# Optimization experiments

Hardware: AMD Instinct MI355X
Metric: run time of the kernel (lower is better)

The kernel has to match this reference:

```python
import jax, jax.numpy as jnp
import numpy as np

STRIDE = 16
HF = WF = 160
IM_H = IM_W = STRIDE * HF  # 2560
A = 15
PRE_NMS = 3000
RPN_KEEP = 300
RPN_NMS_TH = 0.7
OBJ_TH = 0.2
MIN_SIZE = 8.0
G = 7
OUT_DIM = 10
S = 2  # bilinear samples per bin per axis
NUM_FG = 3
SCORE_TH = 0.3
RCNN_NMS_TH = 0.5
FINAL_KEEP = 100
BBOX_STD = jnp.array([0.1, 0.1, 0.2, 0.2], jnp.float32)


def gen_anchors():
    base = 16.0
    anchors = []
    for r in [0.5, 1.0, 2.0]:
        for s in [2.0, 4.0, 8.0, 16.0, 32.0]:
            size = base * s
            w = size * np.sqrt(1.0 / r)
            h = size * np.sqrt(r)
            anchors.append([-w / 2, -h / 2, w / 2, h / 2])
    return jnp.asarray(np.array(anchors, np.float32))  # [A,4]


def decode_boxes(anchors, deltas):
    d = deltas * BBOX_STD
    wa = anchors[..., 2] - anchors[..., 0] + 1.0
    ha = anchors[..., 3] - anchors[..., 1] + 1.0
    cxa = anchors[..., 0] + 0.5 * wa
    cya = anchors[..., 1] + 0.5 * ha
    cx = d[..., 0] * wa + cxa
    cy = d[..., 1] * ha + cya
    w = wa * jnp.exp(jnp.minimum(d[..., 2], 4.0))
    h = ha * jnp.exp(jnp.minimum(d[..., 3], 4.0))
    boxes = jnp.stack([cx - 0.5 * w, cy - 0.5 * h, cx + 0.5 * w, cy + 0.5 * h], -1)
    hi = jnp.array([IM_W - 1.0, IM_H - 1.0, IM_W - 1.0, IM_H - 1.0], jnp.float32)
    return jnp.clip(boxes, 0.0, hi)


def greedy_nms(boxes, scores, iou_th, keep_n):
    # scores <= 0 means pre-suppressed/invalid
    N = boxes.shape[0]
    areas = jnp.maximum(boxes[:, 2] - boxes[:, 0] + 1.0, 0.0) * jnp.maximum(boxes[:, 3] - boxes[:, 1] + 1.0, 0.0)

    def body(k, st):
        sup, keep = st
        s = jnp.where(sup, -1e30, scores)
        i = jnp.argmax(s)
        valid = s[i] > -1e29
        keep = keep.at[k].set(jnp.where(valid, i.astype(jnp.int32), N))
        bi = boxes[i]
        ix1 = jnp.maximum(bi[0], boxes[:, 0]); iy1 = jnp.maximum(bi[1], boxes[:, 1])
        ix2 = jnp.minimum(bi[2], boxes[:, 2]); iy2 = jnp.minimum(bi[3], boxes[:, 3])
        inter = jnp.maximum(ix2 - ix1 + 1.0, 0.0) * jnp.maximum(iy2 - iy1 + 1.0, 0.0)
        iou = inter / jnp.maximum(areas[i] + areas - inter, 1e-6)
        sup2 = (sup | (iou > iou_th)).at[i].set(True)
        sup = jnp.where(valid, sup2, sup)
        return sup, keep

    sup0 = scores <= 0.0
    keep0 = jnp.full((keep_n,), N, jnp.int32)
    _, keep = jax.lax.fori_loop(0, keep_n, body, (sup0, keep0))
    return keep, keep < N


def rpn_proposal(rpn_cls, rpn_bbox):
    fg = rpn_cls[0, A:]                                           # [A,HF,WF] objectness
    deltas = rpn_bbox[0].reshape(A, 4, HF, WF).transpose(0, 2, 3, 1)  # [A,HF,WF,4]
    anchors = gen_anchors()
    sx = jnp.arange(WF, dtype=jnp.float32) * STRIDE
    sy = jnp.arange(HF, dtype=jnp.float32) * STRIDE
    gx, gy = jnp.meshgrid(sx, sy)                                 # [HF,WF]
    shift = jnp.stack([gx, gy, gx, gy], -1)                       # [HF,WF,4]
    all_anchors = anchors[:, None, None, :] + shift[None]         # [A,HF,WF,4]
    boxes = decode_boxes(all_anchors, deltas).reshape(-1, 4)      # [A*HF*WF,4]
    scores = fg.reshape(-1)
    w = boxes[:, 2] - boxes[:, 0] + 1.0
    h = boxes[:, 3] - boxes[:, 1] + 1.0
    ok = (w >= MIN_SIZE) & (h >= MIN_SIZE) & (scores > OBJ_TH)
    scores = jnp.where(ok, scores, 0.0)
    sc, idx = jax.lax.top_k(scores, PRE_NMS)
    bx = boxes[idx]
    keep, valid = greedy_nms(bx, sc, RPN_NMS_TH, RPN_KEEP)
    bxp = jnp.concatenate([bx, jnp.zeros((1, 4), bx.dtype)], 0)
    rois = bxp[keep] * valid[:, None].astype(bx.dtype)            # [RPN_KEEP,4]
    return rois, valid


def psroi_align(ft, rois, valid):
    # ft [490,HF,WF]; position-sensitive channel = (c*G+ph)*G+pw
    x1 = rois[:, 0] / STRIDE; y1 = rois[:, 1] / STRIDE
    x2 = rois[:, 2] / STRIDE; y2 = rois[:, 3] / STRIDE
    bw = jnp.maximum(x2 - x1, 0.1) / G
    bh = jnp.maximum(y2 - y1, 0.1) / G
    frac = (jnp.arange(S, dtype=jnp.float32) + 0.5) / S           # [S]
    grid = jnp.arange(G, dtype=jnp.float32)[None, :, None] + frac[None, None, :]  # [1,G,S]
    ys = jnp.clip(y1[:, None, None] + grid * bh[:, None, None], 0.0, HF - 1.0)    # [R,G,S]
    xs = jnp.clip(x1[:, None, None] + grid * bw[:, None, None], 0.0, WF - 1.0)
    y0 = jnp.floor(ys); x0 = jnp.floor(xs)
    wy = ys - y0; wx = xs - x0
    y0i = y0.astype(jnp.int32); x0i = x0.astype(jnp.int32)
    y1i = jnp.minimum(y0i + 1, HF - 1); x1i = jnp.minimum(x0i + 1, WF - 1)
    chan = (jnp.arange(OUT_DIM)[:, None, None] * G + jnp.arange(G)[None, :, None]) * G + jnp.arange(G)[None, None, :]
    ch = chan[None, :, :, :, None, None]                          # [1,C,G,G,1,1]
    Y0 = y0i[:, None, :, None, :, None]; Y1 = y1i[:, None, :, None, :, None]
    X0 = x0i[:, None, None, :, None, :]; X1 = x1i[:, None, None, :, None, :]
    WY = wy[:, None, :, None, :, None]; WX = wx[:, None, None, :, None, :]
    v00 = ft[ch, Y0, X0]; v01 = ft[ch, Y0, X1]
    v10 = ft[ch, Y1, X0]; v11 = ft[ch, Y1, X1]                    # [R,C,G,G,S,S]
    val = v00 * (1 - WY) * (1 - WX) + v01 * (1 - WY) * WX + v10 * WY * (1 - WX) + v11 * WY * WX
    pooled = val.mean(axis=(4, 5))                                # [R,C,G,G]
    return pooled * valid[:, None, None, None].astype(pooled.dtype)


def rcnn_proposal(cls_sm, bbox_pred, rois, valid):
    R = rois.shape[0]
    deltas = bbox_pred.reshape(R, 4, 4)[:, 1:, :]                 # [R,3,4] fg classes
    boxes = decode_boxes(rois[:, None, :], deltas)                # [R,3,4]
    scores = cls_sm[:, 1:] * valid[:, None].astype(cls_sm.dtype)  # [R,3]
    scores = jnp.where(scores > SCORE_TH, scores, 0.0)
    fb = boxes.reshape(-1, 4)
    fs = scores.reshape(-1)
    labels = jnp.tile(jnp.arange(1, NUM_FG + 1, dtype=jnp.float32), (R,))
    keep, kv = greedy_nms(fb, fs, RCNN_NMS_TH, FINAL_KEEP)
    fbp = jnp.concatenate([fb, jnp.zeros((1, 4), fb.dtype)], 0)
    fsp = jnp.concatenate([fs, jnp.zeros((1,), fs.dtype)], 0)
    flp = jnp.concatenate([labels, jnp.zeros((1,), labels.dtype)], 0)
    out = jnp.concatenate([fbp[keep], fsp[keep][:, None], flp[keep][:, None]], -1)  # [FINAL_KEEP,6]
    return out * kv[:, None].astype(out.dtype)


def setup_inputs() -> dict:
    key = jax.random.key(0)
    ks = jax.random.split(key, 9)
    return {
        'rpn_cls_prob_reshape': jax.random.uniform(ks[0], (1, 2 * A, HF, WF), jnp.float32),
        'rpn_bbox_pred': jax.random.normal(ks[1], (1, 4 * A, HF, WF), jnp.float32),
        'ft_add_left_right': jax.random.normal(ks[2], (1, OUT_DIM * G * G, HF, WF), jnp.float32),
        'w1': jax.random.normal(ks[3], (490, 2048), jnp.float32) * 0.02,
        'b1': jnp.zeros((2048,), jnp.float32),
        'w_cls': jax.random.normal(ks[4], (2048, 4), jnp.float32) * 0.02,
        'b_cls': jnp.zeros((4,), jnp.float32),
        'w_bbox': jax.random.normal(ks[5], (2048, 16), jnp.float32) * 0.02,
        'b_bbox': jnp.zeros((16,), jnp.float32),
    }


def reference(rpn_cls_prob_reshape, rpn_bbox_pred, ft_add_left_right, w1, b1, w_cls, b_cls, w_bbox, b_bbox):
    rois, valid = rpn_proposal(rpn_cls_prob_reshape, rpn_bbox_pred)
    pooled = psroi_align(ft_add_left_right[0], rois, valid)       # [R,10,7,7]
    feats = pooled.reshape(-1, OUT_DIM * G * G)                   # [R,490]
    h = jax.nn.relu(feats @ w1 + b1)
    cls_sm = jax.nn.softmax(h @ w_cls + b_cls, axis=-1)
    bbox = h @ w_bbox + b_bbox
    return rcnn_proposal(cls_sm, bbox, rois, valid)
```

## Files before the change

### kernel.cpp

```cpp
#include <hip/hip_runtime.h>
#include <stdint.h>

#define HF_ 160
#define WF_ 160
#define HFW 25600
#define A_N 15
#define NTOT 384000
#define PRE_N 3000
#define KEEP_N 300
#define FEAT_N 490
#define HID_N 2048
#define RC_N 900
#define FIN_N 100
#define TIE_CAP 1024
#define NW 47
#define NSTAGE 320
#define RNW 15
#define FC1_MT 10
#define FC1_KP 496
#define ZN (65536 * 2 + 32)

__constant__ float c_hw[15] = {
  22.627416997969522f, 45.254833995939045f, 90.509667991878090f, 181.01933598375618f, 362.03867196751236f,
  16.0f, 32.0f, 64.0f, 128.0f, 256.0f,
  11.313708498984761f, 22.627416997969522f, 45.254833995939045f, 90.509667991878090f, 181.01933598375618f
};
__constant__ float c_hh[15] = {
  11.313708498984761f, 22.627416997969522f, 45.254833995939045f, 90.509667991878090f, 181.01933598375618f,
  16.0f, 32.0f, 64.0f, 128.0f, 256.0f,
  22.627416997969522f, 45.254833995939045f, 90.509667991878090f, 181.01933598375618f, 362.03867196751236f
};

__device__ __forceinline__ void decode_one(
    float ax1, float ay1, float ax2, float ay2,
    float dx, float dy, float dw, float dh,
    float& ox1, float& oy1, float& ox2, float& oy2)
{
#pragma clang fp contract(off)
  float wa = (ax2 - ax1) + 1.0f;
  float ha = (ay2 - ay1) + 1.0f;
  float cxa = ax1 + 0.5f * wa;
  float cya = ay1 + 0.5f * ha;
  float d0 = dx * 0.1f;
  float d1 = dy * 0.1f;
  float d2 = dw * 0.2f;
  float d3 = dh * 0.2f;
  float cx = d0 * wa + cxa;
  float cy = d1 * ha + cya;
  float w  = wa * expf(fminf(d2, 4.0f));
  float h  = ha * expf(fminf(d3, 4.0f));
  float x1 = cx - 0.5f * w;
  float y1 = cy - 0.5f * h;
  float x2 = cx + 0.5f * w;
  float y2 = cy + 0.5f * h;
  ox1 = fminf(fmaxf(x1, 0.0f), 2559.0f);
  oy1 = fminf(fmaxf(y1, 0.0f), 2559.0f);
  ox2 = fminf(fmaxf(x2, 0.0f), 2559.0f);
  oy2 = fminf(fmaxf(y2, 0.0f), 2559.0f);
}

__device__ __forceinline__ float iou_ref(
    float ax1, float ay1, float ax2, float ay2, float areaA,
    float bx1, float by1, float bx2, float by2)
{
#pragma clang fp contract(off)
  float ix1 = fmaxf(ax1, bx1);
  float iy1 = fmaxf(ay1, by1);
  float ix2 = fminf(ax2, bx2);
  float iy2 = fminf(ay2, by2);
  float iw = fmaxf((ix2 - ix1) + 1.0f, 0.0f);
  float ih = fmaxf((iy2 - iy1) + 1.0f, 0.0f);
  float inter = iw * ih;
  float areaB = fmaxf((bx2 - bx1) + 1.0f, 0.0f) * fmaxf((by2 - by1) + 1.0f, 0.0f);
  float den = fmaxf(areaA + areaB - inter, 1e-6f);
  return inter / den;
}

__global__ void k_decode_score(const float* __restrict__ cls,
                               const float* __restrict__ bbox,
                               float* __restrict__ scores,
                               uint32_t* __restrict__ histzero)
{
  int e = blockIdx.x * 256 + threadIdx.x;
  if (e < ZN) histzero[e] = 0u;
  if (e >= NTOT) return;
  int a   = e / HFW;
  int rem = e - a * HFW;
  int i   = rem / WF_;
  int j   = rem - i * WF_;
  float score = cls[(A_N + a) * HFW + rem];
  float gx = (float)(j * 16);
  float gy = (float)(i * 16);
  float hw = c_hw[a], hh = c_hh[a];
  float dx = bbox[(a * 4 + 0) * HFW + rem];
  float dy = bbox[(a * 4 + 1) * HFW + rem];
  float dw = bbox[(a * 4 + 2) * HFW + rem];
  float dh = bbox[(a * 4 + 3) * HFW + rem];
  float x1, y1, x2, y2;
  decode_one(gx - hw, gy - hh, gx + hw, gy + hh, dx, dy, dw, dh, x1, y1, x2, y2);
  float bw, bh;
  {
#pragma clang fp contract(off)
    bw = (x2 - x1) + 1.0f;
    bh = (y2 - y1) + 1.0f;
  }
  bool ok = (bw >= 8.0f) && (bh >= 8.0f) && (score > 0.2f);
  scores[e] = ok ? score : 0.0f;
}

__global__ void k_hist_hi(const float* __restrict__ scores, uint32_t* __restrict__ hist)
{
  __shared__ uint32_t lh[512];
  int t = threadIdx.x;
  for (int i = t; i < 512; i += 256) lh[i] = 0u;
  __syncthreads();
  int e = blockIdx.x * 256 + t;
  if (e < NTOT) {
    float s = scores[e];
    if (s > 0.0f) {
      uint32_t b = __float_as_uint(s) >> 16;
      if (b >= 0x3E00u && b < 0x4000u) atomicAdd(&lh[b - 0x3E00u], 1u);
      else atomicAdd(&hist[b], 1u);
    }
  }
  __syncthreads();
  for (int i = t; i < 512; i += 256) {
    uint32_t v = lh[i];
    if (v) atomicAdd(&hist[0x3E00u + i], v);
  }
}

__global__ void __launch_bounds__(1024) k_findbin1(const uint32_t* __restrict__ hist,
                                                   uint32_t* __restrict__ meta)
{
  __shared__ uint32_t sfx[1024];
  __shared__ int s_chunk;
  __shared__ uint32_t s_exc;
  int t = threadIdx.x;
  if (t == 0) s_chunk = -1;
  const uint32_t* hp = hist + t * 64;
  uint32_t s = 0;
#pragma unroll
  for (int b = 0; b < 64; b++) s += hp[b];
  sfx[t] = s;
  __syncthreads();
  for (int d = 1; d < 1024; d <<= 1) {
    uint32_t v = (t + d < 1024) ? sfx[t + d] : 0u;
    __syncthreads();
    sfx[t] += v;
    __syncthreads();
  }
  uint32_t inc = sfx[t];
  uint32_t exc = (t < 1023) ? sfx[t + 1] : 0u;
  if (exc < (uint32_t)PRE_N && inc >= (uint32_t)PRE_N) { s_chunk = t; s_exc = exc; }
  __syncthreads();
  int c = s_chunk;
  if (c < 0) {
    if (t == 0) { meta[0] = 0u; meta[1] = 0u; meta[2] = 1u; }
    return;
  }
  if (t < 64) {
    uint32_t h = hist[c * 64 + t];
    uint32_t v = h;
#pragma unroll
    for (int d = 1; d < 64; d <<= 1) {
      uint32_t o = (uint32_t)__shfl_down((int)v, d);
      v += (t + d < 64) ? o : 0u;
    }
    uint32_t before = s_exc + (v - h);
    if (before < (uint32_t)PRE_N && before + h >= (uint32_t)PRE_N) {
      meta[0] = (uint32_t)(c * 64 + t);
      meta[1] = (uint32_t)PRE_N - before;
      meta[2] = 0u;
    }
  }
}

__global__ void k_hist_lo(const float* __restrict__ scores,
                          const uint32_t* __restrict__ meta,
                          uint32_t* __restrict__ hist2)
{
  if (meta[2]) return;
  uint32_t B1 = meta[0];
  int e = blockIdx.x * 256 + threadIdx.x;
  if (e >= NTOT) return;
  float s = scores[e];
  if (s <= 0.0f) return;
  uint32_t bits = __float_as_uint(s);
  if ((bits >> 16) == B1) atomicAdd(&hist2[bits & 0xFFFFu], 1u);
}

__global__ void __launch_bounds__(1024) k_findT(const uint32_t* __restrict__ hist2,
                                                uint32_t* __restrict__ meta)
{
  if (meta[2]) { if (threadIdx.x == 0) meta[3] = 0u; return; }
  __shared__ uint32_t sfx[1024];
  __shared__ int s_chunk;
  __shared__ uint32_t s_exc;
  int t = threadIdx.x;
  if (t == 0) s_chunk = -1;
  uint32_t K = meta[1];
  const uint32_t* hp = hist2 + t * 64;
  uint32_t s = 0;
#pragma unroll
  for (int b = 0; b < 64; b++) s += hp[b];
  sfx[t] = s;
  __syncthreads();
  for (int d = 1; d < 1024; d <<= 1) {
    uint32_t v = (t + d < 1024) ? sfx[t + d] : 0u;
    __syncthreads();
    sfx[t] += v;
    __syncthreads();
  }
  uint32_t inc = sfx[t];
  uint32_t exc = (t < 1023) ? sfx[t + 1] : 0u;
  if (exc < K && inc >= K) { s_chunk = t; s_exc = exc; }
  __syncthreads();
  int c = s_chunk;
  if (c < 0) { if (t == 0) meta[3] = 0u; return; }
  if (t < 64) {
    uint32_t h = hist2[c * 64 + t];
    uint32_t v = h;
#pragma unroll
    for (int d = 1; d < 64; d <<= 1) {
      uint32_t o = (uint32_t)__shfl_down((int)v, d);
      v += (t + d < 64) ? o : 0u;
    }
    uint32_t before = s_exc + (v - h);
    if (before < K && before + h >= K)
      meta[3] = (meta[0] << 16) | (uint32_t)(c * 64 + t);
  }
}

__global__ void k_compact(const float* __restrict__ scores,
                          const uint32_t* __restrict__ meta,
                          uint64_t* __restrict__ gt,
                          uint64_t* __restrict__ tie,
                          uint32_t* __restrict__ cnts)
{
  int e = blockIdx.x * 256 + threadIdx.x;
  if (e >= NTOT) return;
  float s = scores[e];
  if (s <= 0.0f) return;
  uint32_t bits = __float_as_uint(s);
  uint32_t T = meta[3];
  uint64_t key = ((uint64_t)bits << 32) | (uint32_t)(~(uint32_t)e);
  if (bits > T) {
    uint32_t p = atomicAdd(&cnts[0], 1u);
    if (p < (uint32_t)PRE_N) gt[p] = key;
  } else if (bits == T) {
    uint32_t p = atomicAdd(&cnts[1], 1u);
    if (p < (uint32_t)TIE_CAP) tie[p] = key;
  }
}

__global__ void __launch_bounds__(256) k_rank_gather(
    const uint64_t* __restrict__ gt,
    const uint64_t* __restrict__ tie,
    const uint32_t* __restrict__ cnts,
    const float* __restrict__ bbox,
    float* __restrict__ bxx1, float* __restrict__ bxy1,
    float* __restrict__ bxx2, float* __restrict__ bxy2)
{
  __shared__ uint64_t keys[4096];
  int t = threadIdx.x;
  uint32_t ngt = min(cnts[0], (uint32_t)PRE_N);
  uint32_t nte = min(cnts[1], (uint32_t)TIE_CAP);
  uint32_t M = ngt + nte;
  for (int s = t; s < 4096; s += 256) {
    uint64_t k = 0;
    if ((uint32_t)s < ngt) k = gt[s];
    else if ((uint32_t)s < M) k = tie[s - ngt];
    keys[s] = k;
  }
  __syncthreads();
  int e = blockIdx.x * 256 + t;
  uint64_t my = keys[e];
  if (my == 0) return;
  int r = 0;
#pragma unroll 4
  for (int j = 0; j < 4096; j += 4) {
    uint64_t k0 = keys[j + 0];
    uint64_t k1 = keys[j + 1];
    uint64_t k2 = keys[j + 2];
    uint64_t k3 = keys[j + 3];
    r += (k0 > my) ? 1 : 0;
    r += (k1 > my) ? 1 : 0;
    r += (k2 > my) ? 1 : 0;
    r += (k3 > my) ? 1 : 0;
  }
  if (r >= PRE_N) return;
  int idx = (int)(~(uint32_t)(my & 0xFFFFFFFFull));
  int a   = idx / HFW;
  int rem = idx - a * HFW;
  int i   = rem / WF_;
  int j   = rem - i * WF_;
  float gx = (float)(j * 16);
  float gy = (float)(i * 16);
  float hw = c_hw[a], hh = c_hh[a];
  float dx = bbox[(a * 4 + 0) * HFW + rem];
  float dy = bbox[(a * 4 + 1) * HFW + rem];
  float dw = bbox[(a * 4 + 2) * HFW + rem];
  float dh = bbox[(a * 4 + 3) * HFW + rem];
  float x1, y1, x2, y2;
  decode_one(gx - hw, gy - hh, gx + hw, gy + hh, dx, dy, dw, dh, x1, y1, x2, y2);
  bxx1[r] = x1; bxy1[r] = y1; bxx2[r] = x2; bxy2[r] = y2;
}

__global__ void __launch_bounds__(256) k_iou_mask(
    const float* __restrict__ bxx1, const float* __restrict__ bxy1,
    const float* __restrict__ bxx2, const float* __restrict__ bxy2,
    uint64_t* __restrict__ rowmask, uint64_t* __restrict__ diag)
{
  __shared__ float s1[PRE_N], s2[PRE_N], s3[PRE_N], s4[PRE_N];
  int t = threadIdx.x;
  for (int e = t; e < PRE_N; e += 256) {
    s1[e] = bxx1[e]; s2[e] = bxy1[e]; s3[e] = bxx2[e]; s4[e] = bxy2[e];
  }
  __syncthreads();
  int task = blockIdx.x * 256 + t;
  if (task >= PRE_N * NW) return;
  int row = task / NW;
  int w   = task - row * NW;
  if ((w + 1) * 64 <= row) {
    rowmask[(size_t)row * NW + w] = 0;
    return;
  }
  float ax1 = s1[row], ay1 = s2[row], ax2 = s3[row], ay2 = s4[row];
  float areaA;
  {
#pragma clang fp contract(off)
    areaA = fmaxf((ax2 - ax1) + 1.0f, 0.0f) * fmaxf((ay2 - ay1) + 1.0f, 0.0f);
  }
  int j0 = w << 6;
  uint64_t bits = 0;
  for (int off = 0; off < 64; off++) {
    int jj = (off + t) & 63;
    int j = j0 + jj;
    if (j < PRE_N) {
      float iou = iou_ref(ax1, ay1, ax2, ay2, areaA, s1[j], s2[j], s3[j], s4[j]);
      if (iou > 0.7f) bits |= 1ull << jj;
    }
  }
  rowmask[(size_t)row * NW + w] = bits;
  if (w == (row >> 6)) diag[row] = bits;
}

__global__ void __launch_bounds__(256) k_rpn_scan(
    const float* __restrict__ bxx1, const float* __restrict__ bxy1,
    const float* __restrict__ bxx2, const float* __restrict__ bxy2,
    const uint32_t* __restrict__ cnts,
    const uint64_t* __restrict__ rowmask,
    const uint64_t* __restrict__ diag,
    float* __restrict__ rois, uint32_t* __restrict__ valid)
{
  __shared__ uint64_t rowstage[NSTAGE * NW];
  __shared__ uint64_t sdiag[PRE_N];
  __shared__ int keepIdx[KEEP_N];
  __shared__ int s_nkeep;
  int t = threadIdx.x;
  for (int e = t; e < NSTAGE * NW; e += 256) rowstage[e] = rowmask[e];
  for (int e = t; e < PRE_N; e += 256) sdiag[e] = diag[e];
  __syncthreads();
  if (t < 64) {
    int lane = t;
    uint32_t Mp = min(cnts[0] + min(cnts[1], (uint32_t)TIE_CAP), (uint32_t)PRE_N);
    uint64_t sup = 0, pend = 0;
    int nk = 0;
    int nwords = (int)((Mp + 63u) >> 6);
    for (int w = 0; w < nwords && nk < KEEP_N; w++) {
      sup |= pend; pend = 0;
      uint64_t cw = (uint64_t)__shfl((unsigned long long)sup, w);
      int lim = (int)Mp - (w << 6);
      uint64_t range = (lim >= 64) ? ~0ull : ((1ull << lim) - 1ull);
      uint64_t rem = (~cw) & range;
      while (rem && nk < KEEP_N) {
        int b = __builtin_ctzll(rem);
        int i = (w << 6) + b;
        if (lane == 0) keepIdx[nk] = i;
        nk++;
        uint64_t roww = sdiag[i];
        uint64_t rowl = 0;
        if (lane < NW)
          rowl = (i < NSTAGE) ? rowstage[i * NW + lane]
                              : rowmask[(size_t)i * NW + lane];
        sup |= pend;
        pend = rowl;
        rem &= ~(roww | (1ull << b));
      }
    }
    sup |= pend;
    if (lane == 0) s_nkeep = nk;
  }
  __syncthreads();
  int nk2 = s_nkeep;
  for (int k = t; k < nk2; k += 256) {
    int i = keepIdx[k];
    rois[k * 4 + 0] = bxx1[i];
    rois[k * 4 + 1] = bxy1[i];
    rois[k * 4 + 2] = bxx2[i];
    rois[k * 4 + 3] = bxy2[i];
    valid[k] = 1u;
  }
  for (int e = nk2 * 4 + t; e < KEEP_N * 4; e += 256) rois[e] = 0.0f;
  for (int e = nk2 + t; e < KEEP_N; e += 256) valid[e] = 0u;
}

__global__ void __launch_bounds__(512) k_psroi(const float* __restrict__ ft,
                                               const float* __restrict__ rois,
                                               const uint32_t* __restrict__ valid,
                                               float* __restrict__ feats)
{
#pragma clang fp contract(off)
  int r = blockIdx.x;
  int t = threadIdx.x;
  if (t >= FEAT_N) return;
  float x1 = rois[r * 4 + 0] * 0.0625f;
  float y1 = rois[r * 4 + 1] * 0.0625f;
  float x2 = rois[r * 4 + 2] * 0.0625f;
  float y2 = rois[r * 4 + 3] * 0.0625f;
  float bw = fmaxf(x2 - x1, 0.1f) / 7.0f;
  float bh = fmaxf(y2 - y1, 0.1f) / 7.0f;
  int c   = t / 49;
  int rem = t - c * 49;
  int gy  = rem / 7;
  int gx  = rem - gy * 7;
  (void)c;
  const float* base = ft + t * HFW;
  float acc = 0.0f;
  for (int sy = 0; sy < 2; sy++) {
    float gyf = (float)gy + (sy ? 0.75f : 0.25f);
    float ys = fminf(fmaxf(y1 + gyf * bh, 0.0f), 159.0f);
    float y0f = floorf(ys);
    float wy = ys - y0f;
    int y0 = (int)y0f;
    int y1i = min(y0 + 1, 159);
    for (int sx = 0; sx < 2; sx++) {
      float gxf = (float)gx + (sx ? 0.75f : 0.25f);
      float xs = fminf(fmaxf(x1 + gxf * bw, 0.0f), 159.0f);
      float x0f = floorf(xs);
      float wx = xs - x0f;
      int x0 = (int)x0f;
      int x1i = min(x0 + 1, 159);
      float v00 = base[y0 * WF_ + x0];
      float v01 = base[y0 * WF_ + x1i];
      float v10 = base[y1i * WF_ + x0];
      float v11 = base[y1i * WF_ + x1i];
      float val = v00 * (1.0f - wy) * (1.0f - wx)
                + v01 * (1.0f - wy) * wx
                + v10 * wy * (1.0f - wx)
                + v11 * wy * wx;
      acc += val;
    }
  }
  float pooled = acc * 0.25f;
  feats[r * FEAT_N + t] = valid[r] ? pooled : 0.0f;
}

__global__ void __launch_bounds__(256) k_fc1(const float* __restrict__ feats,
                                             const float* __restrict__ w1,
                                             const float* __restrict__ b1,
                                             float* __restrict__ h)
{
  __shared__ float sf[FC1_MT][FC1_KP];
  int t = threadIdx.x;
  int n = blockIdx.x * 256 + t;
  int m0 = blockIdx.y * FC1_MT;
  for (int idx = t; idx < FC1_MT * FC1_KP; idx += 256) {
    int mm = idx / FC1_KP;
    int kk = idx - mm * FC1_KP;
    sf[mm][kk] = (kk < FEAT_N) ? feats[(m0 + mm) * FEAT_N + kk] : 0.0f;
  }
  __syncthreads();
  float acc[FC1_MT];
#pragma unroll
  for (int i = 0; i < FC1_MT; i++) acc[i] = 0.0f;
  float wb[16];
#pragma unroll
  for (int u = 0; u < 16; u++) wb[u] = w1[u * HID_N + n];
#pragma unroll 1
  for (int kb = 0; kb < FC1_KP - 16; kb += 16) {
    float wn[16];
    int kn = kb + 16;
#pragma unroll
    for (int u = 0; u < 16; u++)
      wn[u] = (kn + u < FEAT_N) ? w1[(kn + u) * HID_N + n] : 0.0f;
#pragma unroll
    for (int u4 = 0; u4 < 4; u4++) {
#pragma unroll
      for (int i = 0; i < FC1_MT; i++) {
        float4 f = *reinterpret_cast<const float4*>(&sf[i][kb + u4 * 4]);
        acc[i] = fmaf(f.x, wb[u4 * 4 + 0], acc[i]);
        acc[i] = fmaf(f.y, wb[u4 * 4 + 1], acc[i]);
        acc[i] = fmaf(f.z, wb[u4 * 4 + 2], acc[i]);
        acc[i] = fmaf(f.w, wb[u4 * 4 + 3], acc[i]);
      }
    }
#pragma unroll
    for (int u = 0; u < 16; u++) wb[u] = wn[u];
  }
  {
    const int kb = FC1_KP - 16;
#pragma unroll
    for (int u4 = 0; u4 < 4; u4++) {
#pragma unroll
      for (int i = 0; i < FC1_MT; i++) {
        float4 f = *reinterpret_cast<const float4*>(&sf[i][kb + u4 * 4]);
        acc[i] = fmaf(f.x, wb[u4 * 4 + 0], acc[i]);
        acc[i] = fmaf(f.y, wb[u4 * 4 + 1], acc[i]);
        acc[i] = fmaf(f.z, wb[u4 * 4 + 2], acc[i]);
        acc[i] = fmaf(f.w, wb[u4 * 4 + 3], acc[i]);
      }
    }
  }
  float b = b1[n];
#pragma unroll
  for (int i = 0; i < FC1_MT; i++) h[(m0 + i) * HID_N + n] = fmaxf(acc[i] + b, 0.0f);
}

__global__ void __launch_bounds__(256) k_fc2(const float* __restrict__ h,
                                             const float* __restrict__ w_cls,
                                             const float* __restrict__ b_cls,
                                             const float* __restrict__ w_bbox,
                                             const float* __restrict__ b_bbox,
                                             const uint32_t* __restrict__ valid,
                                             float* __restrict__ scores3,
                                             float* __restrict__ bbox16)
{
  int r = blockIdx.x;
  int t = threadIdx.x;
  float acc[20];
#pragma unroll
  for (int i = 0; i < 20; i++) acc[i] = 0.0f;
  for (int k = t; k < HID_N; k += 256) {
    float hv = h[r * HID_N + k];
    float4 wc = *reinterpret_cast<const float4*>(w_cls + k * 4);
    acc[0] = fmaf(hv, wc.x, acc[0]);
    acc[1] = fmaf(hv, wc.y, acc[1]);
    acc[2] = fmaf(hv, wc.z, acc[2]);
    acc[3] = fmaf(hv, wc.w, acc[3]);
#pragma unroll
    for (int q = 0; q < 4; q++) {
      float4 wb = *reinterpret_cast<const float4*>(w_bbox + k * 16 + q * 4);
      acc[4 + q * 4 + 0] = fmaf(hv, wb.x, acc[4 + q * 4 + 0]);
      acc[4 + q * 4 + 1] = fmaf(hv, wb.y, acc[4 + q * 4 + 1]);
      acc[4 + q * 4 + 2] = fmaf(hv, wb.z, acc[4 + q * 4 + 2]);
      acc[4 + q * 4 + 3] = fmaf(hv, wb.w, acc[4 + q * 4 + 3]);
    }
  }
#pragma unroll
  for (int off = 32; off > 0; off >>= 1) {
#pragma unroll
    for (int i = 0; i < 20; i++) acc[i] += __shfl_down(acc[i], off);
  }
  __shared__ float red[4][20];
  int wid = t >> 6, lane = t & 63;
  if (lane == 0) {
#pragma unroll
    for (int i = 0; i < 20; i++) red[wid][i] = acc[i];
  }
  __syncthreads();
  if (t == 0) {
    float f[20];
#pragma unroll
    for (int i = 0; i < 20; i++) f[i] = red[0][i] + red[1][i] + red[2][i] + red[3][i];
    float l0 = f[0] + b_cls[0];
    float l1 = f[1] + b_cls[1];
    float l2 = f[2] + b_cls[2];
    float l3 = f[3] + b_cls[3];
    float m = fmaxf(fmaxf(l0, l1), fmaxf(l2, l3));
    float e0 = expf(l0 - m), e1 = expf(l1 - m), e2 = expf(l2 - m), e3 = expf(l3 - m);
    float s = ((e0 + e1) + e2) + e3;
    float vf = valid[r] ? 1.0f : 0.0f;
    scores3[r * 3 + 0] = (e1 / s) * vf;
    scores3[r * 3 + 1] = (e2 / s) * vf;
    scores3[r * 3 + 2] = (e3 / s) * vf;
#pragma unroll
    for (int i = 0; i < 16; i++) bbox16[r * 16 + i] = f[4 + i] + b_bbox[i];
  }
}

__global__ void __launch_bounds__(1024) k_rc_rank(
    const float* __restrict__ rois,
    const float* __restrict__ scores3,
    const float* __restrict__ bbox16,
    float* __restrict__ sx1, float* __restrict__ sy1,
    float* __restrict__ sx2, float* __restrict__ sy2,
    float* __restrict__ ssc, int* __restrict__ sidx,
    uint32_t* __restrict__ rc_meta)
{
  __shared__ uint64_t keys[1024];
  __shared__ int s_npos;
  int t = threadIdx.x;
  if (t == 0) s_npos = 0;
  uint64_t k = 0;
  float x1 = 0.f, y1 = 0.f, x2 = 0.f, y2 = 0.f, sc = 0.f;
  if (t < RC_N) {
    int r = t / 3;
    int c = t - r * 3;
    float ax1 = rois[r * 4 + 0], ay1 = rois[r * 4 + 1];
    float ax2 = rois[r * 4 + 2], ay2 = rois[r * 4 + 3];
    int cb = (c + 1) * 4;
    float dx = bbox16[r * 16 + cb + 0];
    float dy = bbox16[r * 16 + cb + 1];
    float dw = bbox16[r * 16 + cb + 2];
    float dh = bbox16[r * 16 + cb + 3];
    decode_one(ax1, ay1, ax2, ay2, dx, dy, dw, dh, x1, y1, x2, y2);
    sc = scores3[t];
    if (sc > 0.3f)
      k = ((uint64_t)__float_as_uint(sc) << 32) | (uint32_t)(~(uint32_t)t);
  }
  keys[t] = k;
  if (k != 0) atomicAdd(&s_npos, 1);
  __syncthreads();
  if (t == 0) rc_meta[0] = (uint32_t)s_npos;
  if (k == 0) return;
  int r = 0;
#pragma unroll 4
  for (int j = 0; j < 1024; j += 4) {
    uint64_t k0 = keys[j + 0];
    uint64_t k1 = keys[j + 1];
    uint64_t k2 = keys[j + 2];
    uint64_t k3 = keys[j + 3];
    r += (k0 > k) ? 1 : 0;
    r += (k1 > k) ? 1 : 0;
    r += (k2 > k) ? 1 : 0;
    r += (k3 > k) ? 1 : 0;
  }
  sx1[r] = x1; sy1[r] = y1; sx2[r] = x2; sy2[r] = y2;
  ssc[r] = sc; sidx[r] = t;
}

__global__ void __launch_bounds__(256) k_rc_mask(
    const float* __restrict__ sx1, const float* __restrict__ sy1,
    const float* __restrict__ sx2, const float* __restrict__ sy2,
    uint64_t* __restrict__ rcmask, uint64_t* __restrict__ rcdiag)
{
  __shared__ float s1[RC_N], s2[RC_N], s3[RC_N], s4[RC_N];
  int t = threadIdx.x;
  for (int e = t; e < RC_N; e += 256) {
    s1[e] = sx1[e]; s2[e] = sy1[e]; s3[e] = sx2[e]; s4[e] = sy2[e];
  }
  __syncthreads();
  int task = blockIdx.x * 256 + t;
  if (task >= RC_N * RNW) return;
  int row = task / RNW;
  int w   = task - row * RNW;
  if ((w + 1) * 64 <= row) {
    rcmask[(size_t)row * RNW + w] = 0;
    return;
  }
  float ax1 = s1[row], ay1 = s2[row], ax2 = s3[row], ay2 = s4[row];
  float areaA;
  {
#pragma clang fp contract(off)
    areaA = fmaxf((ax2 - ax1) + 1.0f, 0.0f) * fmaxf((ay2 - ay1) + 1.0f, 0.0f);
  }
  int j0 = w << 6;
  uint64_t bits = 0;
  for (int off = 0; off < 64; off++) {
    int jj = (off + t) & 63;
    int j = j0 + jj;
    if (j < RC_N) {
      float iou = iou_ref(ax1, ay1, ax2, ay2, areaA, s1[j], s2[j], s3[j], s4[j]);
      if (iou > 0.5f) bits |= 1ull << jj;
    }
  }
  rcmask[(size_t)row * RNW + w] = bits;
  if (w == (row >> 6)) rcdiag[row] = bits;
}

__global__ void __launch_bounds__(256) k_rc_scan(
    const float* __restrict__ sx1, const float* __restrict__ sy1,
    const float* __restrict__ sx2, const float* __restrict__ sy2,
    const float* __restrict__ ssc, const int* __restrict__ sidx,
    const uint32_t* __restrict__ rc_meta,
    const uint64_t* __restrict__ rcmask,
    const uint64_t* __restrict__ rcdiag,
    float* __restrict__ out)
{
  __shared__ uint64_t rowstage[RC_N * RNW];
  __shared__ uint64_t sdiag[RC_N];
  __shared__ int keepPos[FIN_N];
  __shared__ int s_nk;
  int t = threadIdx.x;
  for (int e = t; e < RC_N * RNW; e += 256) rowstage[e] = rcmask[e];
  for (int e = t; e < RC_N; e += 256) sdiag[e] = rcdiag[e];
  __syncthreads();
  if (t < 64) {
    int lane = t;
    int Npos = (int)min(rc_meta[0], (uint32_t)RC_N);
    uint64_t sup = 0, pend = 0;
    int nk = 0;
    int nwords = (Npos + 63) >> 6;
    for (int w = 0; w < nwords && nk < FIN_N; w++) {
      sup |= pend; pend = 0;
      uint64_t cw = (uint64_t)__shfl((unsigned long long)sup, w);
      int lim = Npos - (w << 6);
      uint64_t range = (lim >= 64) ? ~0ull : ((1ull << lim) - 1ull);
      uint64_t rem = (~cw) & range;
      while (rem && nk < FIN_N) {
        int b = __builtin_ctzll(rem);
        int i = (w << 6) + b;
        if (lane == 0) keepPos[nk] = i;
        nk++;
        uint64_t roww = sdiag[i];
        uint64_t rowl = (lane < RNW) ? rowstage[i * RNW + lane] : 0;
        sup |= pend;
        pend = rowl;
        rem &= ~(roww | (1ull << b));
      }
    }
    sup |= pend;
    if (lane == 0) s_nk = nk;
  }
  __syncthreads();
  int nk = s_nk;
  for (int k = t; k < nk; k += 256) {
    int i = keepPos[k];
    int m = sidx[i];
    out[k * 6 + 0] = sx1[i];
    out[k * 6 + 1] = sy1[i];
    out[k * 6 + 2] = sx2[i];
    out[k * 6 + 3] = sy2[i];
    out[k * 6 + 4] = ssc[i];
    out[k * 6 + 5] = (float)(m - (m / 3) * 3 + 1);
  }
  for (int e = nk * 6 + t; e < FIN_N * 6; e += 256) out[e] = 0.0f;
}

extern "C" void kernel_launch(void* const* d_in, const int* in_sizes, int n_in,
                              void* d_out, int out_size, void* d_ws, size_t ws_size,
                              hipStream_t stream)
{
  (void)in_sizes; (void)n_in; (void)out_size; (void)ws_size;
  const float* rpn_cls  = (const float*)d_in[0];
  const float* rpn_bbox = (const float*)d_in[1];
  const float* ft       = (const float*)d_in[2];
  const float* w1       = (const float*)d_in[3];
  const float* b1       = (const float*)d_in[4];
  const float* w_cls    = (const float*)d_in[5];
  const float* b_cls    = (const float*)d_in[6];
  const float* w_bbox   = (const float*)d_in[7];
  const float* b_bbox   = (const float*)d_in[8];
  float* out = (float*)d_out;

  char* ws = (char*)d_ws;
  size_t off = 0;
  auto alloc = [&](size_t bytes) -> void* {
    void* p = (void*)(ws + off);
    off += (bytes + 15) & ~(size_t)15;
    return p;
  };
  uint32_t* hist1  = (uint32_t*)alloc(65536 * 4);
  uint32_t* hist2  = (uint32_t*)alloc(65536 * 4);
  uint32_t* meta   = (uint32_t*)alloc(32 * 4);
  float*    scores = (float*)alloc((size_t)NTOT * 4);
  uint64_t* gt     = (uint64_t*)alloc(3008 * 8);
  uint64_t* tie    = (uint64_t*)alloc(TIE_CAP * 8);
  float*    bxx1 = (float*)alloc(PRE_N * 4);
  float*    bxy1 = (float*)alloc(PRE_N * 4);
  float*    bxx2 = (float*)alloc(PRE_N * 4);
  float*    bxy2 = (float*)alloc(PRE_N * 4);
  float*    rois  = (float*)alloc(KEEP_N * 4 * 4);
  uint32_t* valid = (uint32_t*)alloc(KEEP_N * 4);
  float*    feats = (float*)alloc((size_t)KEEP_N * FEAT_N * 4);
  float*    hbuf  = (float*)alloc((size_t)KEEP_N * HID_N * 4);
  float*    scores3 = (float*)alloc(RC_N * 4);
  float*    bbox16  = (float*)alloc(KEEP_N * 16 * 4);
  float*    sx1 = (float*)alloc(RC_N * 4);
  float*    sy1 = (float*)alloc(RC_N * 4);
  float*    sx2 = (float*)alloc(RC_N * 4);
  float*    sy2 = (float*)alloc(RC_N * 4);
  float*    ssc = (float*)alloc(RC_N * 4);
  int*      sidx = (int*)alloc(RC_N * 4);
  uint32_t* rc_meta = (uint32_t*)alloc(16 * 4);
  uint64_t* rowmask = (uint64_t*)alloc((size_t)3008 * NW * 8);
  uint64_t* diag    = (uint64_t*)alloc(3008 * 8);
  uint64_t* rcmask  = (uint64_t*)alloc((size_t)RC_N * RNW * 8);
  uint64_t* rcdiag  = (uint64_t*)alloc(904 * 8);

  k_decode_score<<<NTOT / 256, 256, 0, stream>>>(rpn_cls, rpn_bbox, scores, hist1);
  k_hist_hi<<<NTOT / 256, 256, 0, stream>>>(scores, hist1);
  k_findbin1<<<1, 1024, 0, stream>>>(hist1, meta);
  k_hist_lo<<<NTOT / 256, 256, 0, stream>>>(scores, meta, hist2);
  k_findT<<<1, 1024, 0, stream>>>(hist2, meta);
  k_compact<<<NTOT / 256, 256, 0, stream>>>(scores, meta, gt, tie, meta + 8);
  k_rank_gather<<<16, 256, 0, stream>>>(gt, tie, meta + 8, rpn_bbox,
                                        bxx1, bxy1, bxx2, bxy2);
  k_iou_mask<<<(PRE_N * NW + 255) / 256, 256, 0, stream>>>(bxx1, bxy1, bxx2, bxy2,
                                                           rowmask, diag);
  k_rpn_scan<<<1, 256, 0, stream>>>(bxx1, bxy1, bxx2, bxy2, meta + 8,
                                    rowmask, diag, rois, valid);
  k_psroi<<<KEEP_N, 512, 0, stream>>>(ft, rois, valid, feats);
  k_fc1<<<dim3(HID_N / 256, KEEP_N / FC1_MT), 256, 0, stream>>>(feats, w1, b1, hbuf);
  k_fc2<<<KEEP_N, 256, 0, stream>>>(hbuf, w_cls, b_cls, w_bbox, b_bbox, valid,
                                    scores3, bbox16);
  k_rc_rank<<<1, 1024, 0, stream>>>(rois, scores3, bbox16,
                                    sx1, sy1, sx2, sy2, ssc, sidx, rc_meta);
  k_rc_mask<<<(RC_N * RNW + 255) / 256, 256, 0, stream>>>(sx1, sy1, sx2, sy2,
                                                          rcmask, rcdiag);
  k_rc_scan<<<1, 256, 0, stream>>>(sx1, sy1, sx2, sy2, ssc, sidx, rc_meta,
                                   rcmask, rcdiag, out);
}
```

Baseline: 470.6 us.

## Restructure NMS scans to batch row-mask loads per word and split rank kernels

The serial NMS scans now run in a single 64-lane wavefront. They drop the large shared-memory row staging. Within each 64-box word, the diagonal masks are read by shuffle, and the full row masks of kept boxes are loaded later in batches of eight independent global loads rather than one dependent load per kept box. The rank kernels run as more, smaller blocks, and the RPN rank loop stops at the actual key count. The final-stage rank is split from the decode into its own multi-block kernel. This trades an extra launch and extra buffers for shorter serial dependency chains and better parallelism in the single-block stages.

```diff
diff --git a/kernel.cpp b/kernel.cpp
--- a/kernel.cpp
+++ b/kernel.cpp
@@ -14,7 +14,6 @@
 #define FIN_N 100
 #define TIE_CAP 1024
 #define NW 47
-#define NSTAGE 320
 #define RNW 15
 #define FC1_MT 10
 #define FC1_KP 496
@@ -254,7 +253,7 @@
   }
 }
 
-__global__ void __launch_bounds__(256) k_rank_gather(
+__global__ void __launch_bounds__(64) k_rank_gather(
     const uint64_t* __restrict__ gt,
     const uint64_t* __restrict__ tie,
     const uint32_t* __restrict__ cnts,
@@ -267,19 +266,19 @@
   uint32_t ngt = min(cnts[0], (uint32_t)PRE_N);
   uint32_t nte = min(cnts[1], (uint32_t)TIE_CAP);
   uint32_t M = ngt + nte;
-  for (int s = t; s < 4096; s += 256) {
+  for (int s = t; s < 4096; s += 64) {
     uint64_t k = 0;
     if ((uint32_t)s < ngt) k = gt[s];
     else if ((uint32_t)s < M) k = tie[s - ngt];
     keys[s] = k;
   }
   __syncthreads();
-  int e = blockIdx.x * 256 + t;
+  int e = blockIdx.x * 64 + t;
   uint64_t my = keys[e];
   if (my == 0) return;
+  int MM = (int)((M + 3u) & ~3u);
   int r = 0;
-#pragma unroll 4
-  for (int j = 0; j < 4096; j += 4) {
+  for (int j = 0; j < MM; j += 4) {
     uint64_t k0 = keys[j + 0];
     uint64_t k1 = keys[j + 1];
     uint64_t k2 = keys[j + 2];
@@ -346,7 +345,7 @@
   if (w == (row >> 6)) diag[row] = bits;
 }
 
-__global__ void __launch_bounds__(256) k_rpn_scan(
+__global__ void __launch_bounds__(64) k_rpn_scan(
     const float* __restrict__ bxx1, const float* __restrict__ bxy1,
     const float* __restrict__ bxx2, const float* __restrict__ bxy2,
     const uint32_t* __restrict__ cnts,
@@ -354,47 +353,55 @@
     const uint64_t* __restrict__ diag,
     float* __restrict__ rois, uint32_t* __restrict__ valid)
 {
-  __shared__ uint64_t rowstage[NSTAGE * NW];
   __shared__ uint64_t sdiag[PRE_N];
   __shared__ int keepIdx[KEEP_N];
-  __shared__ int s_nkeep;
-  int t = threadIdx.x;
-  for (int e = t; e < NSTAGE * NW; e += 256) rowstage[e] = rowmask[e];
-  for (int e = t; e < PRE_N; e += 256) sdiag[e] = diag[e];
-  __syncthreads();
-  if (t < 64) {
-    int lane = t;
-    uint32_t Mp = min(cnts[0] + min(cnts[1], (uint32_t)TIE_CAP), (uint32_t)PRE_N);
-    uint64_t sup = 0, pend = 0;
-    int nk = 0;
-    int nwords = (int)((Mp + 63u) >> 6);
-    for (int w = 0; w < nwords && nk < KEEP_N; w++) {
-      sup |= pend; pend = 0;
-      uint64_t cw = (uint64_t)__shfl((unsigned long long)sup, w);
-      int lim = (int)Mp - (w << 6);
-      uint64_t range = (lim >= 64) ? ~0ull : ((1ull << lim) - 1ull);
-      uint64_t rem = (~cw) & range;
-      while (rem && nk < KEEP_N) {
-        int b = __builtin_ctzll(rem);
-        int i = (w << 6) + b;
-        if (lane == 0) keepIdx[nk] = i;
-        nk++;
-        uint64_t roww = sdiag[i];
-        uint64_t rowl = 0;
-        if (lane < NW)
-          rowl = (i < NSTAGE) ? rowstage[i * NW + lane]
-                              : rowmask[(size_t)i * NW + lane];
-        sup |= pend;
-        pend = rowl;
-        rem &= ~(roww | (1ull << b));
-      }
-    }
-    sup |= pend;
-    if (lane == 0) s_nkeep = nk;
-  }
-  __syncthreads();
-  int nk2 = s_nkeep;
-  for (int k = t; k < nk2; k += 256) {
+  int lane = threadIdx.x;
+  for (int e = lane; e < PRE_N; e += 64) sdiag[e] = diag[e];
+  __syncthreads();
+  uint32_t Mp = min(cnts[0] + min(cnts[1], (uint32_t)TIE_CAP), (uint32_t)PRE_N);
+  uint64_t sup = 0;
+  int nk = 0;
+  int nwords = (int)((Mp + 63u) >> 6);
+  for (int w = 0; w < nwords && nk < KEEP_N; w++) {
+    uint64_t cw = (uint64_t)__shfl((unsigned long long)sup, w);
+    int ci = (w << 6) + lane;
+    uint64_t dg = (ci < (int)Mp) ? sdiag[ci] : 0;
+    int lim = (int)Mp - (w << 6);
+    uint64_t range = (lim >= 64) ? ~0ull : ((1ull << lim) - 1ull);
+    uint64_t rem = (~cw) & range;
+    uint64_t keepbits = 0;
+    while (rem && nk < KEEP_N) {
+      int b = __builtin_ctzll(rem);
+      keepbits |= 1ull << b;
+      if (lane == 0) keepIdx[nk] = (w << 6) + b;
+      nk++;
+      uint64_t roww = (uint64_t)__shfl((unsigned long long)dg, b);
+      rem &= ~(roww | (1ull << b));
+    }
+    while (keepbits) {
+      uint64_t r0 = 0, r1 = 0, r2 = 0, r3 = 0, r4 = 0, r5 = 0, r6 = 0, r7 = 0;
+      int b;
+      if (keepbits) { b = __builtin_ctzll(keepbits); keepbits &= keepbits - 1;
+        if (lane < NW) r0 = rowmask[(size_t)((w << 6) + b) * NW + lane]; }
+      if (keepbits) { b = __builtin_ctzll(keepbits); keepbits &= keepbits - 1;
+        if (lane < NW) r1 = rowmask[(size_t)((w << 6) + b) * NW + lane]; }
+      if (keepbits) { b = __builtin_ctzll(keepbits); keepbits &= keepbits - 1;
+        if (lane < NW) r2 = rowmask[(size_t)((w << 6) + b) * NW + lane]; }
+      if (keepbits) { b = __builtin_ctzll(keepbits); keepbits &= keepbits - 1;
+        if (lane < NW) r3 = rowmask[(size_t)((w << 6) + b) * NW + lane]; }
+      if (keepbits) { b = __builtin_ctzll(keepbits); keepbits &= keepbits - 1;
+        if (lane < NW) r4 = rowmask[(size_t)((w << 6) + b) * NW + lane]; }
+      if (keepbits) { b = __builtin_ctzll(keepbits); keepbits &= keepbits - 1;
+        if (lane < NW) r5 = rowmask[(size_t)((w << 6) + b) * NW + lane]; }
+      if (keepbits) { b = __builtin_ctzll(keepbits); keepbits &= keepbits - 1;
+        if (lane < NW) r6 = rowmask[(size_t)((w << 6) + b) * NW + lane]; }
+      if (keepbits) { b = __builtin_ctzll(keepbits); keepbits &= keepbits - 1;
+        if (lane < NW) r7 = rowmask[(size_t)((w << 6) + b) * NW + lane]; }
+      sup |= ((r0 | r1) | (r2 | r3)) | ((r4 | r5) | (r6 | r7));
+    }
+  }
+  __syncthreads();
+  for (int k = lane; k < nk; k += 64) {
     int i = keepIdx[k];
     rois[k * 4 + 0] = bxx1[i];
     rois[k * 4 + 1] = bxy1[i];
@@ -402,8 +409,8 @@
     rois[k * 4 + 3] = bxy2[i];
     valid[k] = 1u;
   }
-  for (int e = nk2 * 4 + t; e < KEEP_N * 4; e += 256) rois[e] = 0.0f;
-  for (int e = nk2 + t; e < KEEP_N; e += 256) valid[e] = 0u;
+  for (int e = nk * 4 + lane; e < KEEP_N * 4; e += 64) rois[e] = 0.0f;
+  for (int e = nk + lane; e < KEEP_N; e += 64) valid[e] = 0u;
 }
 
 __global__ void __launch_bounds__(512) k_psroi(const float* __restrict__ ft,
@@ -580,21 +587,19 @@
   }
 }
 
-__global__ void __launch_bounds__(1024) k_rc_rank(
+__global__ void __launch_bounds__(1024) k_rc_decode(
     const float* __restrict__ rois,
     const float* __restrict__ scores3,
     const float* __restrict__ bbox16,
-    float* __restrict__ sx1, float* __restrict__ sy1,
-    float* __restrict__ sx2, float* __restrict__ sy2,
-    float* __restrict__ ssc, int* __restrict__ sidx,
+    float* __restrict__ dbx, float* __restrict__ dby,
+    float* __restrict__ dbX, float* __restrict__ dbY,
+    float* __restrict__ dsc, uint64_t* __restrict__ rckeys,
     uint32_t* __restrict__ rc_meta)
 {
-  __shared__ uint64_t keys[1024];
   __shared__ int s_npos;
   int t = threadIdx.x;
   if (t == 0) s_npos = 0;
   uint64_t k = 0;
-  float x1 = 0.f, y1 = 0.f, x2 = 0.f, y2 = 0.f, sc = 0.f;
   if (t < RC_N) {
     int r = t / 3;
     int c = t - r * 3;
@@ -605,30 +610,48 @@
     float dy = bbox16[r * 16 + cb + 1];
     float dw = bbox16[r * 16 + cb + 2];
     float dh = bbox16[r * 16 + cb + 3];
+    float x1, y1, x2, y2;
     decode_one(ax1, ay1, ax2, ay2, dx, dy, dw, dh, x1, y1, x2, y2);
-    sc = scores3[t];
+    float sc = scores3[t];
+    dbx[t] = x1; dby[t] = y1; dbX[t] = x2; dbY[t] = y2; dsc[t] = sc;
     if (sc > 0.3f)
       k = ((uint64_t)__float_as_uint(sc) << 32) | (uint32_t)(~(uint32_t)t);
   }
-  keys[t] = k;
+  rckeys[t] = k;
   if (k != 0) atomicAdd(&s_npos, 1);
   __syncthreads();
   if (t == 0) rc_meta[0] = (uint32_t)s_npos;
-  if (k == 0) return;
+}
+
+__global__ void __launch_bounds__(64) k_rc_rank2(
+    const uint64_t* __restrict__ rckeys,
+    const float* __restrict__ dbx, const float* __restrict__ dby,
+    const float* __restrict__ dbX, const float* __restrict__ dbY,
+    const float* __restrict__ dsc,
+    float* __restrict__ sx1, float* __restrict__ sy1,
+    float* __restrict__ sx2, float* __restrict__ sy2,
+    float* __restrict__ ssc, int* __restrict__ sidx)
+{
+  __shared__ uint64_t keys[1024];
+  int lane = threadIdx.x;
+  for (int s = lane; s < 1024; s += 64) keys[s] = rckeys[s];
+  __syncthreads();
+  int e = blockIdx.x * 64 + lane;
+  uint64_t my = keys[e];
+  if (my == 0) return;
   int r = 0;
-#pragma unroll 4
   for (int j = 0; j < 1024; j += 4) {
     uint64_t k0 = keys[j + 0];
     uint64_t k1 = keys[j + 1];
     uint64_t k2 = keys[j + 2];
     uint64_t k3 = keys[j + 3];
-    r += (k0 > k) ? 1 : 0;
-    r += (k1 > k) ? 1 : 0;
-    r += (k2 > k) ? 1 : 0;
-    r += (k3 > k) ? 1 : 0;
-  }
-  sx1[r] = x1; sy1[r] = y1; sx2[r] = x2; sy2[r] = y2;
-  ssc[r] = sc; sidx[r] = t;
+    r += (k0 > my) ? 1 : 0;
+    r += (k1 > my) ? 1 : 0;
+    r += (k2 > my) ? 1 : 0;
+    r += (k3 > my) ? 1 : 0;
+  }
+  sx1[r] = dbx[e]; sy1[r] = dby[e]; sx2[r] = dbX[e]; sy2[r] = dbY[e];
+  ssc[r] = dsc[e]; sidx[r] = e;
 }
 
 __global__ void __launch_bounds__(256) k_rc_mask(
@@ -670,7 +693,7 @@
   if (w == (row >> 6)) rcdiag[row] = bits;
 }
 
-__global__ void __launch_bounds__(256) k_rc_scan(
+__global__ void __launch_bounds__(64) k_rc_scan(
     const float* __restrict__ sx1, const float* __restrict__ sy1,
     const float* __restrict__ sx2, const float* __restrict__ sy2,
     const float* __restrict__ ssc, const int* __restrict__ sidx,
@@ -679,44 +702,55 @@
     const uint64_t* __restrict__ rcdiag,
     float* __restrict__ out)
 {
-  __shared__ uint64_t rowstage[RC_N * RNW];
   __shared__ uint64_t sdiag[RC_N];
   __shared__ int keepPos[FIN_N];
-  __shared__ int s_nk;
-  int t = threadIdx.x;
-  for (int e = t; e < RC_N * RNW; e += 256) rowstage[e] = rcmask[e];
-  for (int e = t; e < RC_N; e += 256) sdiag[e] = rcdiag[e];
-  __syncthreads();
-  if (t < 64) {
-    int lane = t;
-    int Npos = (int)min(rc_meta[0], (uint32_t)RC_N);
-    uint64_t sup = 0, pend = 0;
-    int nk = 0;
-    int nwords = (Npos + 63) >> 6;
-    for (int w = 0; w < nwords && nk < FIN_N; w++) {
-      sup |= pend; pend = 0;
-      uint64_t cw = (uint64_t)__shfl((unsigned long long)sup, w);
-      int lim = Npos - (w << 6);
-      uint64_t range = (lim >= 64) ? ~0ull : ((1ull << lim) - 1ull);
-      uint64_t rem = (~cw) & range;
-      while (rem && nk < FIN_N) {
-        int b = __builtin_ctzll(rem);
-        int i = (w << 6) + b;
-        if (lane == 0) keepPos[nk] = i;
-        nk++;
-        uint64_t roww = sdiag[i];
-        uint64_t rowl = (lane < RNW) ? rowstage[i * RNW + lane] : 0;
-        sup |= pend;
-        pend = rowl;
-        rem &= ~(roww | (1ull << b));
-      }
-    }
-    sup |= pend;
-    if (lane == 0) s_nk = nk;
-  }
-  __syncthreads();
-  int nk = s_nk;
-  for (int k = t; k < nk; k += 256) {
+  int lane = threadIdx.x;
+  for (int e = lane; e < RC_N; e += 64) sdiag[e] = rcdiag[e];
+  __syncthreads();
+  int Npos = (int)min(rc_meta[0], (uint32_t)RC_N);
+  uint64_t sup = 0;
+  int nk = 0;
+  int nwords = (Npos + 63) >> 6;
+  for (int w = 0; w < nwords && nk < FIN_N; w++) {
+    uint64_t cw = (uint64_t)__shfl((unsigned long long)sup, w);
+    int ci = (w << 6) + lane;
+    uint64_t dg = (ci < Npos) ? sdiag[ci] : 0;
+    int lim = Npos - (w << 6);
+    uint64_t range = (lim >= 64) ? ~0ull : ((1ull << lim) - 1ull);
+    uint64_t rem = (~cw) & range;
+    uint64_t keepbits = 0;
+    while (rem && nk < FIN_N) {
+      int b = __builtin_ctzll(rem);
+      keepbits |= 1ull << b;
+      if (lane == 0) keepPos[nk] = (w << 6) + b;
+      nk++;
+      uint64_t roww = (uint64_t)__shfl((unsigned long long)dg, b);
+      rem &= ~(roww | (1ull << b));
+    }
+    while (keepbits) {
+      uint64_t r0 = 0, r1 = 0, r2 = 0, r3 = 0, r4 = 0, r5 = 0, r6 = 0, r7 = 0;
+      int b;
+      if (keepbits) { b = __builtin_ctzll(keepbits); keepbits &= keepbits - 1;
+        if (lane < RNW) r0 = rcmask[(size_t)((w << 6) + b) * RNW + lane]; }
+      if (keepbits) { b = __builtin_ctzll(keepbits); keepbits &= keepbits - 1;
+        if (lane < RNW) r1 = rcmask[(size_t)((w << 6) + b) * RNW + lane]; }
+      if (keepbits) { b = __builtin_ctzll(keepbits); keepbits &= keepbits - 1;
+        if (lane < RNW) r2 = rcmask[(size_t)((w << 6) + b) * RNW + lane]; }
+      if (keepbits) { b = __builtin_ctzll(keepbits); keepbits &= keepbits - 1;
+        if (lane < RNW) r3 = rcmask[(size_t)((w << 6) + b) * RNW + lane]; }
+      if (keepbits) { b = __builtin_ctzll(keepbits); keepbits &= keepbits - 1;
+        if (lane < RNW) r4 = rcmask[(size_t)((w << 6) + b) * RNW + lane]; }
+      if (keepbits) { b = __builtin_ctzll(keepbits); keepbits &= keepbits - 1;
+        if (lane < RNW) r5 = rcmask[(size_t)((w << 6) + b) * RNW + lane]; }
+      if (keepbits) { b = __builtin_ctzll(keepbits); keepbits &= keepbits - 1;
+        if (lane < RNW) r6 = rcmask[(size_t)((w << 6) + b) * RNW + lane]; }
+      if (keepbits) { b = __builtin_ctzll(keepbits); keepbits &= keepbits - 1;
+        if (lane < RNW) r7 = rcmask[(size_t)((w << 6) + b) * RNW + lane]; }
+      sup |= ((r0 | r1) | (r2 | r3)) | ((r4 | r5) | (r6 | r7));
+    }
+  }
+  __syncthreads();
+  for (int k = lane; k < nk; k += 64) {
     int i = keepPos[k];
     int m = sidx[i];
     out[k * 6 + 0] = sx1[i];
@@ -726,7 +760,7 @@
     out[k * 6 + 4] = ssc[i];
     out[k * 6 + 5] = (float)(m - (m / 3) * 3 + 1);
   }
-  for (int e = nk * 6 + t; e < FIN_N * 6; e += 256) out[e] = 0.0f;
+  for (int e = nk * 6 + lane; e < FIN_N * 6; e += 64) out[e] = 0.0f;
 }
 
 extern "C" void kernel_launch(void* const* d_in, const int* in_sizes, int n_in,
@@ -775,6 +809,12 @@
   float*    ssc = (float*)alloc(RC_N * 4);
   int*      sidx = (int*)alloc(RC_N * 4);
   uint32_t* rc_meta = (uint32_t*)alloc(16 * 4);
+  float*    dbx = (float*)alloc(RC_N * 4);
+  float*    dby = (float*)alloc(RC_N * 4);
+  float*    dbX = (float*)alloc(RC_N * 4);
+  float*    dbY = (float*)alloc(RC_N * 4);
+  float*    dsc = (float*)alloc(RC_N * 4);
+  uint64_t* rckeys = (uint64_t*)alloc(1024 * 8);
   uint64_t* rowmask = (uint64_t*)alloc((size_t)3008 * NW * 8);
   uint64_t* diag    = (uint64_t*)alloc(3008 * 8);
   uint64_t* rcmask  = (uint64_t*)alloc((size_t)RC_N * RNW * 8);
@@ -786,20 +826,22 @@
   k_hist_lo<<<NTOT / 256, 256, 0, stream>>>(scores, meta, hist2);
   k_findT<<<1, 1024, 0, stream>>>(hist2, meta);
   k_compact<<<NTOT / 256, 256, 0, stream>>>(scores, meta, gt, tie, meta + 8);
-  k_rank_gather<<<16, 256, 0, stream>>>(gt, tie, meta + 8, rpn_bbox,
-                                        bxx1, bxy1, bxx2, bxy2);
+  k_rank_gather<<<63, 64, 0, stream>>>(gt, tie, meta + 8, rpn_bbox,
+                                       bxx1, bxy1, bxx2, bxy2);
   k_iou_mask<<<(PRE_N * NW + 255) / 256, 256, 0, stream>>>(bxx1, bxy1, bxx2, bxy2,
                                                            rowmask, diag);
-  k_rpn_scan<<<1, 256, 0, stream>>>(bxx1, bxy1, bxx2, bxy2, meta + 8,
-                                    rowmask, diag, rois, valid);
+  k_rpn_scan<<<1, 64, 0, stream>>>(bxx1, bxy1, bxx2, bxy2, meta + 8,
+                                   rowmask, diag, rois, valid);
   k_psroi<<<KEEP_N, 512, 0, stream>>>(ft, rois, valid, feats);
   k_fc1<<<dim3(HID_N / 256, KEEP_N / FC1_MT), 256, 0, stream>>>(feats, w1, b1, hbuf);
   k_fc2<<<KEEP_N, 256, 0, stream>>>(hbuf, w_cls, b_cls, w_bbox, b_bbox, valid,
                                     scores3, bbox16);
-  k_rc_rank<<<1, 1024, 0, stream>>>(rois, scores3, bbox16,
-                                    sx1, sy1, sx2, sy2, ssc, sidx, rc_meta);
+  k_rc_decode<<<1, 1024, 0, stream>>>(rois, scores3, bbox16,
+                                      dbx, dby, dbX, dbY, dsc, rckeys, rc_meta);
+  k_rc_rank2<<<15, 64, 0, stream>>>(rckeys, dbx, dby, dbX, dbY, dsc,
+                                    sx1, sy1, sx2, sy2, ssc, sidx);
   k_rc_mask<<<(RC_N * RNW + 255) / 256, 256, 0, stream>>>(sx1, sy1, sx2, sy2,
                                                           rcmask, rcdiag);
-  k_rc_scan<<<1, 256, 0, stream>>>(sx1, sy1, sx2, sy2, ssc, sidx, rc_meta,
-                                   rcmask, rcdiag, out);
-}
+  k_rc_scan<<<1, 64, 0, stream>>>(sx1, sy1, sx2, sy2, ssc, sidx, rc_meta,
+                                  rcmask, rcdiag, out);
+}
```

After: 450.6 us. 1.04x faster.
